# Optimization experiments

Hardware: AMD Instinct MI355X
Metric: run time of the kernel (lower is better)

The kernel has to match this reference:

```python
import jax, jax.numpy as jnp
import numpy as np

D_MODEL = 1024
NHEAD = 16
HEAD_DIM = D_MODEL // NHEAD
D_FF = 4096
EPS = 1e-5


def _layernorm(x, g, b):
    mu = jnp.mean(x, axis=-1, keepdims=True)
    var = jnp.mean((x - mu) ** 2, axis=-1, keepdims=True)
    return (x - mu) * jax.lax.rsqrt(var + EPS) * g + b


def setup_inputs() -> dict:
    key = jax.random.key(0)
    ks = jax.random.split(key, 13)
    s = 1.0 / np.sqrt(D_MODEL)
    sf = 1.0 / np.sqrt(D_FF)
    # weights stored as [in, out] (transposed torch Linear)
    return {
        "src": jax.random.normal(ks[0], (4, 2048, D_MODEL), jnp.float32),
        "Wq": jax.random.uniform(ks[1], (D_MODEL, D_MODEL), jnp.float32, -s, s),
        "bq": jnp.zeros((D_MODEL,), jnp.float32),
        "Wk": jax.random.uniform(ks[2], (D_MODEL, D_MODEL), jnp.float32, -s, s),
        "bk": jnp.zeros((D_MODEL,), jnp.float32),
        "Wv": jax.random.uniform(ks[3], (D_MODEL, D_MODEL), jnp.float32, -s, s),
        "bv": jnp.zeros((D_MODEL,), jnp.float32),
        "Wo": jax.random.uniform(ks[4], (D_MODEL, D_MODEL), jnp.float32, -s, s),
        "bo": jnp.zeros((D_MODEL,), jnp.float32),
        "W1": jax.random.uniform(ks[5], (D_MODEL, D_FF), jnp.float32, -s, s),
        "b1": jnp.zeros((D_FF,), jnp.float32),
        "W2": jax.random.uniform(ks[6], (D_FF, D_MODEL), jnp.float32, -sf, sf),
        "b2": jnp.zeros((D_MODEL,), jnp.float32),
        "g1": jnp.ones((D_MODEL,), jnp.float32),
        "be1": jnp.zeros((D_MODEL,), jnp.float32),
        "g2": jnp.ones((D_MODEL,), jnp.float32),
        "be2": jnp.zeros((D_MODEL,), jnp.float32),
    }


def reference(src, Wq, bq, Wk, bk, Wv, bv, Wo, bo, W1, b1, W2, b2, g1, be1, g2, be2):
    B, S, _ = src.shape
    scale = 1.0 / np.sqrt(HEAD_DIM)
    # project and split heads: [B, H, S, Dh]
    def heads(W, b):
        return (src @ W + b).reshape(B, S, NHEAD, HEAD_DIM).transpose(0, 2, 1, 3)
    Q, K, V = heads(Wq, bq), heads(Wk, bk), heads(Wv, bv)
    scores = jnp.einsum('bhqd,bhkd->bhqk', Q, K) * scale
    attn = jax.nn.softmax(scores, axis=-1)
    ctx = jnp.einsum('bhqk,bhkd->bhqd', attn, V)
    ctx = ctx.transpose(0, 2, 1, 3).reshape(B, S, D_MODEL)
    attn_out = ctx @ Wo + bo
    x = _layernorm(src + attn_out, g1, be1)
    ff = jax.nn.relu(x @ W1 + b1) @ W2 + b2
    return _layernorm(x + ff, g2, be2)
```

## Files before the change

kernel.cpp:

```cpp
#include <hip/hip_runtime.h>

typedef __attribute__((ext_vector_type(8))) short bf16x8;
typedef __attribute__((ext_vector_type(4))) float f32x4;
typedef unsigned short u16;
typedef unsigned int u32;

__device__ __forceinline__ u16 f2b(float f) {
  u32 u = __float_as_uint(f);
  u = (u + 0x7fffu + ((u >> 16) & 1u)) >> 16;
  return (u16)u;
}
__device__ __forceinline__ float b2f(u16 b) {
  return __uint_as_float(((u32)b) << 16);
}
__device__ __forceinline__ u32 cvtpk_bf16(float lo, float hi) {
  u32 r;
  asm("v_cvt_pk_bf16_f32 %0, %1, %2" : "=v"(r) : "v"(lo), "v"(hi));
  return r;
}
__device__ __forceinline__ void gload_lds16(const u16* g, u16* l) {
  __builtin_amdgcn_global_load_lds(
      (const __attribute__((address_space(1))) void*)g,
      (__attribute__((address_space(3))) void*)l, 16, 0, 0);
}

__global__ __launch_bounds__(256) void cvt_bf16(const float* __restrict__ in,
                                                u16* __restrict__ out, int n4) {
  int i = blockIdx.x * 256 + threadIdx.x;
  if (i >= n4) return;
  float4 v = ((const float4*)in)[i];
  ushort4 o;
  o.x = f2b(v.x); o.y = f2b(v.y); o.z = f2b(v.z); o.w = f2b(v.w);
  ((ushort4*)out)[i] = o;
}

__global__ __launch_bounds__(256) void transpose_w(const float* __restrict__ in,
                                                   u16* __restrict__ out,
                                                   int R, int C) {
  __shared__ float t[32][33];
  int tid = threadIdx.x, tx = tid & 31, ty = tid >> 5;
  int rb = blockIdx.y * 32, cb = blockIdx.x * 32;
  for (int i = 0; i < 4; i++)
    t[ty + i * 8][tx] = in[(size_t)(rb + ty + i * 8) * C + cb + tx];
  __syncthreads();
  for (int i = 0; i < 4; i++)
    out[(size_t)(cb + ty + i * 8) * R + rb + tx] = f2b(t[tx][ty + i * 8]);
}

__global__ __launch_bounds__(256) void concat3(const float* __restrict__ a,
                                               const float* __restrict__ b,
                                               const float* __restrict__ c,
                                               float* __restrict__ o) {
  int i = blockIdx.x * 256 + threadIdx.x;
  if (i >= 3072) return;
  o[i] = i < 1024 ? a[i] : (i < 2048 ? b[i - 1024] : c[i - 2048]);
}

__device__ __forceinline__ void stage_quarter(const u16* __restrict__ src,
                                              size_t rowbase, int K, int kcol,
                                              u16* dst, int c, int srow, int sg,
                                              int wid) {
  int row_ = c * 64 + srow;
  int gs_ = sg ^ (row_ & 7);
  gload_lds16(src + (rowbase + row_) * K + kcol + gs_ * 8,
              &dst[(c * 64 + wid * 8) * 64]);
}

template <bool PF>
__device__ __forceinline__ void tile_step(
    const u16* sAc, const u16* sBc, u16* sAn, u16* sBn,
    const u16* __restrict__ A, const u16* __restrict__ Bt, size_t abase,
    size_t bbase, int K, int Tn, int wm, int wn, int l16, int lq, int srow,
    int sg, int wid, f32x4 (&acc)[8][4]) {
  __syncthreads();
#pragma unroll
  for (int ks = 0; ks < 2; ++ks) {
    bf16x8 Bf[4], Af[4];
#pragma unroll
    for (int j = 0; j < 4; ++j) {
      int r = wn * 64 + j * 16 + l16;
      Bf[j] = *(const bf16x8*)&sBc[r * 64 + (((ks * 4 + lq) ^ (r & 7)) << 3)];
    }
#pragma unroll
    for (int i = 0; i < 4; ++i) {
      int r = wm * 128 + i * 16 + l16;
      Af[i] = *(const bf16x8*)&sAc[r * 64 + (((ks * 4 + lq) ^ (r & 7)) << 3)];
    }
    if (PF) {
      const u16* src = (ks == 0) ? A : Bt;
      size_t rb = (ks == 0) ? abase : bbase;
      u16* dst = (ks == 0) ? sAn : sBn;
      stage_quarter(src, rb, K, Tn * 64, dst, 0, srow, sg, wid);
      stage_quarter(src, rb, K, Tn * 64, dst, 1, srow, sg, wid);
    }
    __builtin_amdgcn_s_setprio(1);
#pragma unroll
    for (int i = 0; i < 4; ++i)
#pragma unroll
      for (int j = 0; j < 4; ++j)
        acc[i][j] = __builtin_amdgcn_mfma_f32_16x16x32_bf16(Af[i], Bf[j],
                                                            acc[i][j], 0, 0, 0);
    __builtin_amdgcn_s_setprio(0);
#pragma unroll
    for (int i = 0; i < 4; ++i) {
      int r = wm * 128 + 64 + i * 16 + l16;
      Af[i] = *(const bf16x8*)&sAc[r * 64 + (((ks * 4 + lq) ^ (r & 7)) << 3)];
    }
    if (PF) {
      const u16* src = (ks == 0) ? A : Bt;
      size_t rb = (ks == 0) ? abase : bbase;
      u16* dst = (ks == 0) ? sAn : sBn;
      stage_quarter(src, rb, K, Tn * 64, dst, 2, srow, sg, wid);
      stage_quarter(src, rb, K, Tn * 64, dst, 3, srow, sg, wid);
    }
    __builtin_amdgcn_s_setprio(1);
#pragma unroll
    for (int i = 0; i < 4; ++i)
#pragma unroll
      for (int j = 0; j < 4; ++j)
        acc[4 + i][j] = __builtin_amdgcn_mfma_f32_16x16x32_bf16(
            Af[i], Bf[j], acc[4 + i][j], 0, 0, 0);
    __builtin_amdgcn_s_setprio(0);
  }
}

template <int MODE>
__global__ __launch_bounds__(512, 1) void gemm256(const u16* __restrict__ A,
                                                  const u16* __restrict__ Bt,
                                                  const float* __restrict__ bias,
                                                  void* __restrict__ out,
                                                  int M, int N, int K,
                                                  float oscale) {
  __shared__ u16 sA0[256 * 64];
  __shared__ u16 sB0[256 * 64];
  __shared__ u16 sA1[256 * 64];
  __shared__ u16 sB1[256 * 64];
  const int tid = threadIdx.x, lane = tid & 63, wid = tid >> 6;
  const int l16 = lane & 15, lq = lane >> 4;
  const int wm = wid >> 2, wn = wid & 3;
  const size_t abase = (size_t)blockIdx.x * 256;
  const size_t bbase = (size_t)blockIdx.y * 256;
  const int srow = tid >> 3;
  const int sg = tid & 7;
  const int nt = K >> 6;

  f32x4 acc[8][4];
#pragma unroll
  for (int i = 0; i < 8; ++i)
#pragma unroll
    for (int j = 0; j < 4; ++j) acc[i][j] = (f32x4){0.f, 0.f, 0.f, 0.f};

#pragma unroll
  for (int c = 0; c < 4; ++c) {
    stage_quarter(A, abase, K, 0, sA0, c, srow, sg, wid);
    stage_quarter(Bt, bbase, K, 0, sB0, c, srow, sg, wid);
  }

  int T = 0;
  for (; T + 2 < nt; T += 2) {
    tile_step<true>(sA0, sB0, sA1, sB1, A, Bt, abase, bbase, K, T + 1, wm, wn,
                    l16, lq, srow, sg, wid, acc);
    tile_step<true>(sA1, sB1, sA0, sB0, A, Bt, abase, bbase, K, T + 2, wm, wn,
                    l16, lq, srow, sg, wid, acc);
  }
  tile_step<true>(sA0, sB0, sA1, sB1, A, Bt, abase, bbase, K, nt - 1, wm, wn,
                  l16, lq, srow, sg, wid, acc);
  tile_step<false>(sA1, sB1, sA0, sB0, A, Bt, abase, bbase, K, 0, wm, wn, l16,
                   lq, srow, sg, wid, acc);

  const int gmb = blockIdx.x * 256 + wm * 128;
  const int gnb = blockIdx.y * 256 + wn * 64;
#pragma unroll
  for (int i = 0; i < 8; ++i) {
    int gm0 = gmb + i * 16 + lq * 4;
#pragma unroll
    for (int j = 0; j < 4; ++j) {
      int gn = gnb + j * 16 + l16;
      float bv = bias[gn];
#pragma unroll
      for (int r = 0; r < 4; ++r) {
        float v = acc[i][j][r] + bv;
        ((u16*)out)[(size_t)(gm0 + r) * N + gn] = f2b(v > 0.f ? v : 0.f);
      }
    }
  }
}

template <bool PF>
__device__ __forceinline__ void tile_stepR(
    const u16* sAc, const u16* sBc, u16* sAn, u16* sBn,
    const u16* __restrict__ A, const u16* __restrict__ Bt, size_t abase,
    size_t bbase, int K, int Tn, int wm, int wn, int l16, int lq, int srow,
    int sg, int wid, f32x4 (&acc)[4][4]) {
  __syncthreads();
#pragma unroll
  for (int ks = 0; ks < 2; ++ks) {
    bf16x8 Bf[4], Af[4];
#pragma unroll
    for (int j = 0; j < 4; ++j) {
      int r = wn * 64 + j * 16 + l16;
      Bf[j] = *(const bf16x8*)&sBc[r * 64 + (((ks * 4 + lq) ^ (r & 7)) << 3)];
    }
#pragma unroll
    for (int i = 0; i < 4; ++i) {
      int r = wm * 64 + i * 16 + l16;
      Af[i] = *(const bf16x8*)&sAc[r * 64 + (((ks * 4 + lq) ^ (r & 7)) << 3)];
    }
    if (PF) {
      if (ks == 0) {
        stage_quarter(A, abase, K, Tn * 64, sAn, 0, srow, sg, wid);
        stage_quarter(A, abase, K, Tn * 64, sAn, 1, srow, sg, wid);
        stage_quarter(Bt, bbase, K, Tn * 64, sBn, 0, srow, sg, wid);
      } else {
        stage_quarter(Bt, bbase, K, Tn * 64, sBn, 1, srow, sg, wid);
        stage_quarter(Bt, bbase, K, Tn * 64, sBn, 2, srow, sg, wid);
        stage_quarter(Bt, bbase, K, Tn * 64, sBn, 3, srow, sg, wid);
      }
    }
    __builtin_amdgcn_s_setprio(1);
#pragma unroll
    for (int i = 0; i < 4; ++i)
#pragma unroll
      for (int j = 0; j < 4; ++j)
        acc[i][j] = __builtin_amdgcn_mfma_f32_16x16x32_bf16(Af[i], Bf[j],
                                                            acc[i][j], 0, 0, 0);
    __builtin_amdgcn_s_setprio(0);
  }
}

template <int MODE>
__global__ __launch_bounds__(512, 1) void gemmR(const u16* __restrict__ A,
                                                const u16* __restrict__ Bt,
                                                const float* __restrict__ bias,
                                                void* __restrict__ out,
                                                int M, int N, int K,
                                                float oscale) {
  __shared__ u16 sA0[128 * 64];
  __shared__ u16 sB0[256 * 64];
  __shared__ u16 sA1[128 * 64];
  __shared__ u16 sB1[256 * 64];
  const int tid = threadIdx.x, lane = tid & 63, wid = tid >> 6;
  const int l16 = lane & 15, lq = lane >> 4;
  const int wm = wid >> 2, wn = wid & 3;
  const size_t abase = (size_t)blockIdx.x * 128;
  const size_t bbase = (size_t)blockIdx.y * 256;
  const int srow = tid >> 3;
  const int sg = tid & 7;
  const int nt = K >> 6;

  f32x4 acc[4][4];
#pragma unroll
  for (int i = 0; i < 4; ++i)
#pragma unroll
    for (int j = 0; j < 4; ++j) acc[i][j] = (f32x4){0.f, 0.f, 0.f, 0.f};

#pragma unroll
  for (int c = 0; c < 2; ++c) stage_quarter(A, abase, K, 0, sA0, c, srow, sg, wid);
#pragma unroll
  for (int c = 0; c < 4; ++c) stage_quarter(Bt, bbase, K, 0, sB0, c, srow, sg, wid);

  int T = 0;
  for (; T + 2 < nt; T += 2) {
    tile_stepR<true>(sA0, sB0, sA1, sB1, A, Bt, abase, bbase, K, T + 1, wm, wn,
                     l16, lq, srow, sg, wid, acc);
    tile_stepR<true>(sA1, sB1, sA0, sB0, A, Bt, abase, bbase, K, T + 2, wm, wn,
                     l16, lq, srow, sg, wid, acc);
  }
  tile_stepR<true>(sA0, sB0, sA1, sB1, A, Bt, abase, bbase, K, nt - 1, wm, wn,
                   l16, lq, srow, sg, wid, acc);
  tile_stepR<false>(sA1, sB1, sA0, sB0, A, Bt, abase, bbase, K, 0, wm, wn, l16,
                    lq, srow, sg, wid, acc);

  const int gmb = blockIdx.x * 128 + wm * 64;
  const int gnb = blockIdx.y * 256 + wn * 64;
#pragma unroll
  for (int i = 0; i < 4; ++i) {
    int gm0 = gmb + i * 16 + lq * 4;
#pragma unroll
    for (int j = 0; j < 4; ++j) {
      int gn = gnb + j * 16 + l16;
      float bv = bias[gn];
      if constexpr (MODE == 1) {
#pragma unroll
        for (int r = 0; r < 4; ++r)
          ((u16*)out)[(size_t)(gm0 + r) * N + gn] = f2b(acc[i][j][r] + bv);
      } else {
        int sel = gn >> 10;
        int h = (gn & 1023) >> 6, d = gn & 63;
        int b = gm0 >> 11, s = gm0 & 2047;
        u16* o = (u16*)out + (size_t)sel * (8u << 20);
        if (sel == 2) {
          ushort4 w;
          w.x = f2b(acc[i][j][0] + bv);
          w.y = f2b(acc[i][j][1] + bv);
          w.z = f2b(acc[i][j][2] + bv);
          w.w = f2b(acc[i][j][3] + bv);
          *(ushort4*)(o + ((size_t)((b * 16 + h) * 64 + d)) * 2048 + s) = w;
        } else {
          float sc = (sel == 0) ? oscale : 1.f;
#pragma unroll
          for (int r = 0; r < 4; ++r)
            o[((size_t)(b * 16 + h) * 2048 + s + r) * 64 + d] =
                f2b((acc[i][j][r] + bv) * sc);
        }
      }
    }
  }
}

__global__ __launch_bounds__(256) void attn_fwd(const u16* __restrict__ Q,
                                                const u16* __restrict__ Kb,
                                                const u16* __restrict__ Vt,
                                                u16* __restrict__ ctx) {
  __shared__ u16 sK[64][64];
  __shared__ u16 sV[64][64];
  __shared__ u16 sP[4][16][72];
  const int tid = threadIdx.x, lane = tid & 63, wid = tid >> 6;
  const int l16 = lane & 15, lq = lane >> 4;
  const int bh = blockIdx.y, qt = blockIdx.x;
  const size_t base = (size_t)bh * (2048 * 64);
  const int xk = l16 & 7;

  bf16x8 qf[2];
  {
    int qrow = qt * 64 + wid * 16 + l16;
    qf[0] = *(const bf16x8*)(Q + base + (size_t)qrow * 64 + lq * 8);
    qf[1] = *(const bf16x8*)(Q + base + (size_t)qrow * 64 + 32 + lq * 8);
  }
  f32x4 o[4];
#pragma unroll
  for (int j = 0; j < 4; j++) o[j] = (f32x4){0.f, 0.f, 0.f, 0.f};
  float lrow = 0.f;

  const int srow_c = lane >> 3;
  const int sg8 = ((lane & 7) ^ srow_c) * 8;
  const int row0 = wid * 16 + srow_c, row1 = row0 + 8;
  const int wslot = (lane & 7) * 8;

  const u16* kp0 = Kb + base + (size_t)row0 * 64 + sg8;
  const u16* kp1 = Kb + base + (size_t)row1 * 64 + sg8;
  const u16* vp0 = Vt + base + (size_t)row0 * 2048 + sg8;
  const u16* vp1 = Vt + base + (size_t)row1 * 2048 + sg8;

  uint4 rk0 = *(const uint4*)kp0;
  uint4 rk1 = *(const uint4*)kp1;
  uint4 rv0 = *(const uint4*)vp0;
  uint4 rv1 = *(const uint4*)vp1;

  for (int kv0 = 0; kv0 < 2048; kv0 += 64) {
    __syncthreads();
    *(uint4*)&sK[row0][wslot] = rk0;
    *(uint4*)&sK[row1][wslot] = rk1;
    *(uint4*)&sV[row0][wslot] = rv0;
    *(uint4*)&sV[row1][wslot] = rv1;
    if (kv0 + 64 < 2048) {
      int kn = kv0 + 64;
      rk0 = *(const uint4*)(kp0 + (size_t)kn * 64);
      rk1 = *(const uint4*)(kp1 + (size_t)kn * 64);
      rv0 = *(const uint4*)(vp0 + kn);
      rv1 = *(const uint4*)(vp1 + kn);
    }
    __syncthreads();

    f32x4 sf[4];
#pragma unroll
    for (int j = 0; j < 4; j++) sf[j] = (f32x4){0.f, 0.f, 0.f, 0.f};
    __builtin_amdgcn_s_setprio(1);
#pragma unroll
    for (int ks = 0; ks < 2; ks++)
#pragma unroll
      for (int j = 0; j < 4; j++) {
        bf16x8 kf = *(const bf16x8*)&sK[j * 16 + l16][((ks * 4 + lq) ^ xk) * 8];
        sf[j] = __builtin_amdgcn_mfma_f32_16x16x32_bf16(kf, qf[ks], sf[j], 0, 0, 0);
      }
    __builtin_amdgcn_s_setprio(0);

    float rs = 0.f;
#pragma unroll
    for (int j = 0; j < 4; j++) {
      float p0 = __builtin_amdgcn_exp2f(sf[j][0]);
      float p1 = __builtin_amdgcn_exp2f(sf[j][1]);
      float p2 = __builtin_amdgcn_exp2f(sf[j][2]);
      float p3 = __builtin_amdgcn_exp2f(sf[j][3]);
      rs += (p0 + p1) + (p2 + p3);
      uint2 w;
      w.x = cvtpk_bf16(p0, p1);
      w.y = cvtpk_bf16(p2, p3);
      *(uint2*)&sP[wid][l16][j * 16 + lq * 4] = w;
    }
    rs += __shfl_xor(rs, 16);
    rs += __shfl_xor(rs, 32);
    lrow += rs;

    __builtin_amdgcn_s_setprio(1);
#pragma unroll
    for (int ks = 0; ks < 2; ks++) {
      bf16x8 pf = *(const bf16x8*)&sP[wid][l16][ks * 32 + lq * 8];
#pragma unroll
      for (int j = 0; j < 4; j++) {
        bf16x8 vf = *(const bf16x8*)&sV[j * 16 + l16][((ks * 4 + lq) ^ xk) * 8];
        o[j] = __builtin_amdgcn_mfma_f32_16x16x32_bf16(pf, vf, o[j], 0, 0, 0);
      }
    }
    __builtin_amdgcn_s_setprio(0);
  }

  float lval[4];
#pragma unroll
  for (int r = 0; r < 4; r++) lval[r] = 1.f / __shfl(lrow, lq * 4 + r);
  const int b = bh >> 4, h = bh & 15;
#pragma unroll
  for (int j = 0; j < 4; j++)
#pragma unroll
    for (int r = 0; r < 4; r++) {
      int srow = qt * 64 + wid * 16 + lq * 4 + r;
      int d = j * 16 + l16;
      ctx[((size_t)(b * 2048 + srow)) * 1024 + h * 64 + d] = f2b(o[j][r] * lval[r]);
    }
}

template <int A_BF16, int B_BF16, int WRITE_F32>
__global__ __launch_bounds__(256) void ln_res(const void* __restrict__ a,
                                              const void* __restrict__ bsrc,
                                              const float* __restrict__ g,
                                              const float* __restrict__ be,
                                              float* __restrict__ outf,
                                              u16* __restrict__ outb) {
  const int row = blockIdx.x, tid = threadIdx.x;
  const size_t off = (size_t)row * 1024 + tid * 4;
  float4 x;
  if constexpr (A_BF16) {
    ushort4 av = *(const ushort4*)((const u16*)a + off);
    x.x = b2f(av.x); x.y = b2f(av.y); x.z = b2f(av.z); x.w = b2f(av.w);
  } else {
    x = *(const float4*)((const float*)a + off);
  }
  if constexpr (B_BF16) {
    ushort4 bv = *(const ushort4*)((const u16*)bsrc + off);
    x.x += b2f(bv.x); x.y += b2f(bv.y); x.z += b2f(bv.z); x.w += b2f(bv.w);
  } else {
    float4 bb = *(const float4*)((const float*)bsrc + off);
    x.x += bb.x; x.y += bb.y; x.z += bb.z; x.w += bb.w;
  }
  float s = x.x + x.y + x.z + x.w;
  float s2 = x.x * x.x + x.y * x.y + x.z * x.z + x.w * x.w;
  for (int o = 1; o < 64; o <<= 1) {
    s += __shfl_xor(s, o);
    s2 += __shfl_xor(s2, o);
  }
  __shared__ float rbuf[8];
  int lane = tid & 63, wid = tid >> 6;
  if (lane == 0) { rbuf[wid] = s; rbuf[4 + wid] = s2; }
  __syncthreads();
  s = rbuf[0] + rbuf[1] + rbuf[2] + rbuf[3];
  s2 = rbuf[4] + rbuf[5] + rbuf[6] + rbuf[7];
  float mu = s * (1.f / 1024.f);
  float var = s2 * (1.f / 1024.f) - mu * mu;
  float rstd = rsqrtf(var + 1e-5f);
  int c = tid * 4;
  float y0 = (x.x - mu) * rstd * g[c + 0] + be[c + 0];
  float y1 = (x.y - mu) * rstd * g[c + 1] + be[c + 1];
  float y2 = (x.z - mu) * rstd * g[c + 2] + be[c + 2];
  float y3 = (x.w - mu) * rstd * g[c + 3] + be[c + 3];
  if constexpr (WRITE_F32) {
    float4 y; y.x = y0; y.y = y1; y.z = y2; y.w = y3;
    *(float4*)(outf + off) = y;
  } else {
    ushort4 yb;
    yb.x = f2b(y0); yb.y = f2b(y1); yb.z = f2b(y2); yb.w = f2b(y3);
    *(ushort4*)(outb + off) = yb;
  }
}

extern "C" void kernel_launch(void* const* d_in, const int* in_sizes, int n_in,
                              void* d_out, int out_size, void* d_ws, size_t ws_size,
                              hipStream_t stream) {
  const float* src = (const float*)d_in[0];
  const float* Wq = (const float*)d_in[1];
  const float* bq = (const float*)d_in[2];
  const float* Wk = (const float*)d_in[3];
  const float* bk = (const float*)d_in[4];
  const float* Wv = (const float*)d_in[5];
  const float* bv = (const float*)d_in[6];
  const float* Wo = (const float*)d_in[7];
  const float* bo = (const float*)d_in[8];
  const float* W1 = (const float*)d_in[9];
  const float* b1 = (const float*)d_in[10];
  const float* W2 = (const float*)d_in[11];
  const float* b2 = (const float*)d_in[12];
  const float* g1 = (const float*)d_in[13];
  const float* be1 = (const float*)d_in[14];
  const float* g2 = (const float*)d_in[15];
  const float* be2 = (const float*)d_in[16];
  float* out = (float*)d_out;
  char* ws = (char*)d_ws;
  const size_t MB = 1ull << 20;

  u16* XB    = (u16*)(ws + 0);
  u16* WQKVT = (u16*)(ws + 16 * MB);
  u16* WOT   = (u16*)(ws + 22 * MB);
  u16* W1T   = (u16*)(ws + 24 * MB);
  u16* W2T   = (u16*)(ws + 32 * MB);
  float* bqkv = (float*)(ws + 40 * MB);
  u16* Qb    = (u16*)(ws + 41 * MB);
  u16* Kbuf  = (u16*)(ws + 57 * MB);
  u16* Vt    = (u16*)(ws + 73 * MB);
  u16* CTX   = XB;
  u16* AO    = (u16*)(ws + 41 * MB);
  u16* H1    = (u16*)(ws + 57 * MB);
  u16* XBUF  = (u16*)(ws + 121 * MB);
  u16* FF    = XB;

  const float QSCALE = 0.125f * 1.44269504088896340736f;

  cvt_bf16<<<dim3(8192), dim3(256), 0, stream>>>(src, XB, 2097152);
  transpose_w<<<dim3(32, 32), dim3(256), 0, stream>>>(Wq, WQKVT, 1024, 1024);
  transpose_w<<<dim3(32, 32), dim3(256), 0, stream>>>(Wk, WQKVT + 1024 * 1024, 1024, 1024);
  transpose_w<<<dim3(32, 32), dim3(256), 0, stream>>>(Wv, WQKVT + 2048 * 1024, 1024, 1024);
  transpose_w<<<dim3(32, 32), dim3(256), 0, stream>>>(Wo, WOT, 1024, 1024);
  transpose_w<<<dim3(128, 32), dim3(256), 0, stream>>>(W1, W1T, 1024, 4096);
  transpose_w<<<dim3(32, 128), dim3(256), 0, stream>>>(W2, W2T, 4096, 1024);
  concat3<<<dim3(12), dim3(256), 0, stream>>>(bq, bk, bv, bqkv);

  gemmR<6><<<dim3(64, 12), dim3(512), 0, stream>>>(XB, WQKVT, bqkv, Qb,
                                                   8192, 3072, 1024, QSCALE);
  attn_fwd<<<dim3(32, 64), dim3(256), 0, stream>>>(Qb, Kbuf, Vt, CTX);
  gemmR<1><<<dim3(64, 4), dim3(512), 0, stream>>>(CTX, WOT, bo, AO,
                                                  8192, 1024, 1024, 1.0f);
  ln_res<0, 1, 0><<<dim3(8192), dim3(256), 0, stream>>>(src, AO, g1, be1, nullptr, XBUF);
  gemm256<2><<<dim3(32, 16), dim3(512), 0, stream>>>(XBUF, W1T, b1, H1,
                                                     8192, 4096, 1024, 1.0f);
  gemmR<1><<<dim3(64, 4), dim3(512), 0, stream>>>(H1, W2T, b2, FF,
                                                  8192, 1024, 4096, 1.0f);
  ln_res<1, 1, 1><<<dim3(8192), dim3(256), 0, stream>>>(XBUF, FF, g2, be2, out, nullptr);
}
```

Measured before the change: 367.6 us.

## Switch GEMMs to 4-stage BK=32 LDS pipeline with explicit vmcnt waits

```diff
diff --git a/kernel.cpp b/kernel.cpp
--- a/kernel.cpp
+++ b/kernel.cpp
@@ -22,6 +22,21 @@
   __builtin_amdgcn_global_load_lds(
       (const __attribute__((address_space(1))) void*)g,
       (__attribute__((address_space(3))) void*)l, 16, 0, 0);
+}
+template <int N>
+__device__ __forceinline__ void wait_vm_barrier() {
+  if constexpr (N == 8) asm volatile("s_waitcnt vmcnt(8)" ::: "memory");
+  else if constexpr (N == 6) asm volatile("s_waitcnt vmcnt(6)" ::: "memory");
+  else if constexpr (N == 4) asm volatile("s_waitcnt vmcnt(4)" ::: "memory");
+  else if constexpr (N == 3) asm volatile("s_waitcnt vmcnt(3)" ::: "memory");
+  else asm volatile("s_waitcnt vmcnt(0)" ::: "memory");
+  __builtin_amdgcn_s_barrier();
+  asm volatile("" ::: "memory");
+}
+__device__ __forceinline__ void align_barrier() {
+  asm volatile("" ::: "memory");
+  __builtin_amdgcn_s_barrier();
+  asm volatile("" ::: "memory");
 }
 
 __global__ __launch_bounds__(256) void cvt_bf16(const float* __restrict__ in,
@@ -56,72 +71,63 @@
   o[i] = i < 1024 ? a[i] : (i < 2048 ? b[i - 1024] : c[i - 2048]);
 }
 
-__device__ __forceinline__ void stage_quarter(const u16* __restrict__ src,
-                                              size_t rowbase, int K, int kcol,
-                                              u16* dst, int c, int srow, int sg,
-                                              int wid) {
-  int row_ = c * 64 + srow;
-  int gs_ = sg ^ (row_ & 7);
+__device__ __forceinline__ void stage32(const u16* __restrict__ src,
+                                        size_t rowbase, int K, int kcol,
+                                        u16* dst, int c, int tid) {
+  int row_ = c * 128 + (tid >> 2);
+  int gs_ = (tid & 3) ^ (row_ & 3);
   gload_lds16(src + (rowbase + row_) * K + kcol + gs_ * 8,
-              &dst[(c * 64 + wid * 8) * 64]);
+              &dst[(c * 128 + (tid >> 6) * 16) * 32]);
 }
 
 template <bool PF>
-__device__ __forceinline__ void tile_step(
-    const u16* sAc, const u16* sBc, u16* sAn, u16* sBn,
+__device__ __forceinline__ void tile32_256(
+    const u16* pA, const u16* pB, u16* wA, u16* wB,
     const u16* __restrict__ A, const u16* __restrict__ Bt, size_t abase,
-    size_t bbase, int K, int Tn, int wm, int wn, int l16, int lq, int srow,
-    int sg, int wid, f32x4 (&acc)[8][4]) {
-  __syncthreads();
-#pragma unroll
-  for (int ks = 0; ks < 2; ++ks) {
-    bf16x8 Bf[4], Af[4];
-#pragma unroll
-    for (int j = 0; j < 4; ++j) {
-      int r = wn * 64 + j * 16 + l16;
-      Bf[j] = *(const bf16x8*)&sBc[r * 64 + (((ks * 4 + lq) ^ (r & 7)) << 3)];
-    }
-#pragma unroll
-    for (int i = 0; i < 4; ++i) {
-      int r = wm * 128 + i * 16 + l16;
-      Af[i] = *(const bf16x8*)&sAc[r * 64 + (((ks * 4 + lq) ^ (r & 7)) << 3)];
-    }
-    if (PF) {
-      const u16* src = (ks == 0) ? A : Bt;
-      size_t rb = (ks == 0) ? abase : bbase;
-      u16* dst = (ks == 0) ? sAn : sBn;
-      stage_quarter(src, rb, K, Tn * 64, dst, 0, srow, sg, wid);
-      stage_quarter(src, rb, K, Tn * 64, dst, 1, srow, sg, wid);
-    }
-    __builtin_amdgcn_s_setprio(1);
-#pragma unroll
-    for (int i = 0; i < 4; ++i)
-#pragma unroll
-      for (int j = 0; j < 4; ++j)
-        acc[i][j] = __builtin_amdgcn_mfma_f32_16x16x32_bf16(Af[i], Bf[j],
-                                                            acc[i][j], 0, 0, 0);
-    __builtin_amdgcn_s_setprio(0);
-#pragma unroll
-    for (int i = 0; i < 4; ++i) {
-      int r = wm * 128 + 64 + i * 16 + l16;
-      Af[i] = *(const bf16x8*)&sAc[r * 64 + (((ks * 4 + lq) ^ (r & 7)) << 3)];
-    }
-    if (PF) {
-      const u16* src = (ks == 0) ? A : Bt;
-      size_t rb = (ks == 0) ? abase : bbase;
-      u16* dst = (ks == 0) ? sAn : sBn;
-      stage_quarter(src, rb, K, Tn * 64, dst, 2, srow, sg, wid);
-      stage_quarter(src, rb, K, Tn * 64, dst, 3, srow, sg, wid);
-    }
-    __builtin_amdgcn_s_setprio(1);
-#pragma unroll
-    for (int i = 0; i < 4; ++i)
-#pragma unroll
-      for (int j = 0; j < 4; ++j)
-        acc[4 + i][j] = __builtin_amdgcn_mfma_f32_16x16x32_bf16(
-            Af[i], Bf[j], acc[4 + i][j], 0, 0, 0);
-    __builtin_amdgcn_s_setprio(0);
-  }
+    size_t bbase, int K, int Tn, int wm, int wn, int l16, int lq, int tid,
+    f32x4 (&acc)[8][4]) {
+  bf16x8 Bf[4], Af[4];
+#pragma unroll
+  for (int j = 0; j < 4; ++j) {
+    int r = wn * 64 + j * 16 + l16;
+    Bf[j] = *(const bf16x8*)&pB[r * 32 + ((lq ^ (r & 3)) << 3)];
+  }
+#pragma unroll
+  for (int i = 0; i < 4; ++i) {
+    int r = wm * 128 + i * 16 + l16;
+    Af[i] = *(const bf16x8*)&pA[r * 32 + ((lq ^ (r & 3)) << 3)];
+  }
+  if (PF) {
+    stage32(A, abase, K, Tn * 32, wA, 0, tid);
+    stage32(A, abase, K, Tn * 32, wA, 1, tid);
+  }
+  align_barrier();
+  __builtin_amdgcn_s_setprio(1);
+#pragma unroll
+  for (int i = 0; i < 4; ++i)
+#pragma unroll
+    for (int j = 0; j < 4; ++j)
+      acc[i][j] = __builtin_amdgcn_mfma_f32_16x16x32_bf16(Af[i], Bf[j],
+                                                          acc[i][j], 0, 0, 0);
+  __builtin_amdgcn_s_setprio(0);
+#pragma unroll
+  for (int i = 0; i < 4; ++i) {
+    int r = wm * 128 + 64 + i * 16 + l16;
+    Af[i] = *(const bf16x8*)&pA[r * 32 + ((lq ^ (r & 3)) << 3)];
+  }
+  if (PF) {
+    stage32(Bt, bbase, K, Tn * 32, wB, 0, tid);
+    stage32(Bt, bbase, K, Tn * 32, wB, 1, tid);
+  }
+  align_barrier();
+  __builtin_amdgcn_s_setprio(1);
+#pragma unroll
+  for (int i = 0; i < 4; ++i)
+#pragma unroll
+    for (int j = 0; j < 4; ++j)
+      acc[4 + i][j] = __builtin_amdgcn_mfma_f32_16x16x32_bf16(
+          Af[i], Bf[j], acc[4 + i][j], 0, 0, 0);
+  __builtin_amdgcn_s_setprio(0);
 }
 
 template <int MODE>
@@ -131,18 +137,14 @@
                                                   void* __restrict__ out,
                                                   int M, int N, int K,
                                                   float oscale) {
-  __shared__ u16 sA0[256 * 64];
-  __shared__ u16 sB0[256 * 64];
-  __shared__ u16 sA1[256 * 64];
-  __shared__ u16 sB1[256 * 64];
+  __shared__ u16 sA0[256 * 32], sA1[256 * 32], sA2[256 * 32], sA3[256 * 32];
+  __shared__ u16 sB0[256 * 32], sB1[256 * 32], sB2[256 * 32], sB3[256 * 32];
   const int tid = threadIdx.x, lane = tid & 63, wid = tid >> 6;
   const int l16 = lane & 15, lq = lane >> 4;
   const int wm = wid >> 2, wn = wid & 3;
   const size_t abase = (size_t)blockIdx.x * 256;
   const size_t bbase = (size_t)blockIdx.y * 256;
-  const int srow = tid >> 3;
-  const int sg = tid & 7;
-  const int nt = K >> 6;
+  const int nt = K >> 5;
 
   f32x4 acc[8][4];
 #pragma unroll
@@ -150,23 +152,35 @@
 #pragma unroll
     for (int j = 0; j < 4; ++j) acc[i][j] = (f32x4){0.f, 0.f, 0.f, 0.f};
 
-#pragma unroll
-  for (int c = 0; c < 4; ++c) {
-    stage_quarter(A, abase, K, 0, sA0, c, srow, sg, wid);
-    stage_quarter(Bt, bbase, K, 0, sB0, c, srow, sg, wid);
-  }
-
-  int T = 0;
-  for (; T + 2 < nt; T += 2) {
-    tile_step<true>(sA0, sB0, sA1, sB1, A, Bt, abase, bbase, K, T + 1, wm, wn,
-                    l16, lq, srow, sg, wid, acc);
-    tile_step<true>(sA1, sB1, sA0, sB0, A, Bt, abase, bbase, K, T + 2, wm, wn,
-                    l16, lq, srow, sg, wid, acc);
-  }
-  tile_step<true>(sA0, sB0, sA1, sB1, A, Bt, abase, bbase, K, nt - 1, wm, wn,
-                  l16, lq, srow, sg, wid, acc);
-  tile_step<false>(sA1, sB1, sA0, sB0, A, Bt, abase, bbase, K, 0, wm, wn, l16,
-                   lq, srow, sg, wid, acc);
+  stage32(A, abase, K, 0, sA0, 0, tid);
+  stage32(A, abase, K, 0, sA0, 1, tid);
+  stage32(Bt, bbase, K, 0, sB0, 0, tid);
+  stage32(Bt, bbase, K, 0, sB0, 1, tid);
+  stage32(A, abase, K, 32, sA1, 0, tid);
+  stage32(A, abase, K, 32, sA1, 1, tid);
+  stage32(Bt, bbase, K, 32, sB1, 0, tid);
+  stage32(Bt, bbase, K, 32, sB1, 1, tid);
+  stage32(A, abase, K, 64, sA2, 0, tid);
+  stage32(A, abase, K, 64, sA2, 1, tid);
+  stage32(Bt, bbase, K, 64, sB2, 0, tid);
+  stage32(Bt, bbase, K, 64, sB2, 1, tid);
+
+  u16 *A0 = sA0, *A1 = sA1, *A2 = sA2, *A3 = sA3;
+  u16 *B0 = sB0, *B1 = sB1, *B2 = sB2, *B3 = sB3;
+  for (int T = 0; T < nt; ++T) {
+    if (T < nt - 2) wait_vm_barrier<8>();
+    else if (T == nt - 2) wait_vm_barrier<4>();
+    else wait_vm_barrier<0>();
+    if (T + 3 < nt)
+      tile32_256<true>(A0, B0, A3, B3, A, Bt, abase, bbase, K, T + 3, wm, wn,
+                       l16, lq, tid, acc);
+    else
+      tile32_256<false>(A0, B0, A3, B3, A, Bt, abase, bbase, K, 0, wm, wn, l16,
+                        lq, tid, acc);
+    u16* t;
+    t = A0; A0 = A1; A1 = A2; A2 = A3; A3 = t;
+    t = B0; B0 = B1; B1 = B2; B2 = B3; B3 = t;
+  }
 
   const int gmb = blockIdx.x * 256 + wm * 128;
   const int gnb = blockIdx.y * 256 + wn * 64;
@@ -187,45 +201,36 @@
 }
 
 template <bool PF>
-__device__ __forceinline__ void tile_stepR(
-    const u16* sAc, const u16* sBc, u16* sAn, u16* sBn,
+__device__ __forceinline__ void tile32_R(
+    const u16* pA, const u16* pB, u16* wA, u16* wB,
     const u16* __restrict__ A, const u16* __restrict__ Bt, size_t abase,
-    size_t bbase, int K, int Tn, int wm, int wn, int l16, int lq, int srow,
-    int sg, int wid, f32x4 (&acc)[4][4]) {
-  __syncthreads();
-#pragma unroll
-  for (int ks = 0; ks < 2; ++ks) {
-    bf16x8 Bf[4], Af[4];
-#pragma unroll
-    for (int j = 0; j < 4; ++j) {
-      int r = wn * 64 + j * 16 + l16;
-      Bf[j] = *(const bf16x8*)&sBc[r * 64 + (((ks * 4 + lq) ^ (r & 7)) << 3)];
-    }
-#pragma unroll
-    for (int i = 0; i < 4; ++i) {
-      int r = wm * 64 + i * 16 + l16;
-      Af[i] = *(const bf16x8*)&sAc[r * 64 + (((ks * 4 + lq) ^ (r & 7)) << 3)];
-    }
-    if (PF) {
-      if (ks == 0) {
-        stage_quarter(A, abase, K, Tn * 64, sAn, 0, srow, sg, wid);
-        stage_quarter(A, abase, K, Tn * 64, sAn, 1, srow, sg, wid);
-        stage_quarter(Bt, bbase, K, Tn * 64, sBn, 0, srow, sg, wid);
-      } else {
-        stage_quarter(Bt, bbase, K, Tn * 64, sBn, 1, srow, sg, wid);
-        stage_quarter(Bt, bbase, K, Tn * 64, sBn, 2, srow, sg, wid);
-        stage_quarter(Bt, bbase, K, Tn * 64, sBn, 3, srow, sg, wid);
-      }
-    }
-    __builtin_amdgcn_s_setprio(1);
-#pragma unroll
-    for (int i = 0; i < 4; ++i)
-#pragma unroll
-      for (int j = 0; j < 4; ++j)
-        acc[i][j] = __builtin_amdgcn_mfma_f32_16x16x32_bf16(Af[i], Bf[j],
-                                                            acc[i][j], 0, 0, 0);
-    __builtin_amdgcn_s_setprio(0);
-  }
+    size_t bbase, int K, int Tn, int wm, int wn, int l16, int lq, int tid,
+    f32x4 (&acc)[4][4]) {
+  bf16x8 Bf[4], Af[4];
+#pragma unroll
+  for (int j = 0; j < 4; ++j) {
+    int r = wn * 64 + j * 16 + l16;
+    Bf[j] = *(const bf16x8*)&pB[r * 32 + ((lq ^ (r & 3)) << 3)];
+  }
+#pragma unroll
+  for (int i = 0; i < 4; ++i) {
+    int r = wm * 64 + i * 16 + l16;
+    Af[i] = *(const bf16x8*)&pA[r * 32 + ((lq ^ (r & 3)) << 3)];
+  }
+  if (PF) {
+    stage32(A, abase, K, Tn * 32, wA, 0, tid);
+    stage32(Bt, bbase, K, Tn * 32, wB, 0, tid);
+    stage32(Bt, bbase, K, Tn * 32, wB, 1, tid);
+  }
+  align_barrier();
+  __builtin_amdgcn_s_setprio(1);
+#pragma unroll
+  for (int i = 0; i < 4; ++i)
+#pragma unroll
+    for (int j = 0; j < 4; ++j)
+      acc[i][j] = __builtin_amdgcn_mfma_f32_16x16x32_bf16(Af[i], Bf[j],
+                                                          acc[i][j], 0, 0, 0);
+  __builtin_amdgcn_s_setprio(0);
 }
 
 template <int MODE>
@@ -235,18 +240,14 @@
                                                 void* __restrict__ out,
                                                 int M, int N, int K,
                                                 float oscale) {
-  __shared__ u16 sA0[128 * 64];
-  __shared__ u16 sB0[256 * 64];
-  __shared__ u16 sA1[128 * 64];
-  __shared__ u16 sB1[256 * 64];
+  __shared__ u16 sA0[128 * 32], sA1[128 * 32], sA2[128 * 32], sA3[128 * 32];
+  __shared__ u16 sB0[256 * 32], sB1[256 * 32], sB2[256 * 32], sB3[256 * 32];
   const int tid = threadIdx.x, lane = tid & 63, wid = tid >> 6;
   const int l16 = lane & 15, lq = lane >> 4;
   const int wm = wid >> 2, wn = wid & 3;
   const size_t abase = (size_t)blockIdx.x * 128;
   const size_t bbase = (size_t)blockIdx.y * 256;
-  const int srow = tid >> 3;
-  const int sg = tid & 7;
-  const int nt = K >> 6;
+  const int nt = K >> 5;
 
   f32x4 acc[4][4];
 #pragma unroll
@@ -254,22 +255,32 @@
 #pragma unroll
     for (int j = 0; j < 4; ++j) acc[i][j] = (f32x4){0.f, 0.f, 0.f, 0.f};
 
-#pragma unroll
-  for (int c = 0; c < 2; ++c) stage_quarter(A, abase, K, 0, sA0, c, srow, sg, wid);
-#pragma unroll
-  for (int c = 0; c < 4; ++c) stage_quarter(Bt, bbase, K, 0, sB0, c, srow, sg, wid);
-
-  int T = 0;
-  for (; T + 2 < nt; T += 2) {
-    tile_stepR<true>(sA0, sB0, sA1, sB1, A, Bt, abase, bbase, K, T + 1, wm, wn,
-                     l16, lq, srow, sg, wid, acc);
-    tile_stepR<true>(sA1, sB1, sA0, sB0, A, Bt, abase, bbase, K, T + 2, wm, wn,
-                     l16, lq, srow, sg, wid, acc);
-  }
-  tile_stepR<true>(sA0, sB0, sA1, sB1, A, Bt, abase, bbase, K, nt - 1, wm, wn,
-                   l16, lq, srow, sg, wid, acc);
-  tile_stepR<false>(sA1, sB1, sA0, sB0, A, Bt, abase, bbase, K, 0, wm, wn, l16,
-                    lq, srow, sg, wid, acc);
+  stage32(A, abase, K, 0, sA0, 0, tid);
+  stage32(Bt, bbase, K, 0, sB0, 0, tid);
+  stage32(Bt, bbase, K, 0, sB0, 1, tid);
+  stage32(A, abase, K, 32, sA1, 0, tid);
+  stage32(Bt, bbase, K, 32, sB1, 0, tid);
+  stage32(Bt, bbase, K, 32, sB1, 1, tid);
+  stage32(A, abase, K, 64, sA2, 0, tid);
+  stage32(Bt, bbase, K, 64, sB2, 0, tid);
+  stage32(Bt, bbase, K, 64, sB2, 1, tid);
+
+  u16 *A0 = sA0, *A1 = sA1, *A2 = sA2, *A3 = sA3;
+  u16 *B0 = sB0, *B1 = sB1, *B2 = sB2, *B3 = sB3;
+  for (int T = 0; T < nt; ++T) {
+    if (T < nt - 2) wait_vm_barrier<6>();
+    else if (T == nt - 2) wait_vm_barrier<3>();
+    else wait_vm_barrier<0>();
+    if (T + 3 < nt)
+      tile32_R<true>(A0, B0, A3, B3, A, Bt, abase, bbase, K, T + 3, wm, wn,
+                     l16, lq, tid, acc);
+    else
+      tile32_R<false>(A0, B0, A3, B3, A, Bt, abase, bbase, K, 0, wm, wn, l16,
+                      lq, tid, acc);
+    u16* t;
+    t = A0; A0 = A1; A1 = A2; A2 = A3; A3 = t;
+    t = B0; B0 = B1; B1 = B2; B2 = B3; B3 = t;
+  }
 
   const int gmb = blockIdx.x * 128 + wm * 64;
   const int gnb = blockIdx.y * 256 + wn * 64;
```

New measurement: 928.8 us. +152.7%, slower.

## Restructure GEMM main loop into 4-phase schedule with partial vmcnt barriers

Applied to the files above, without the earlier changes.

```diff
diff --git a/kernel.cpp b/kernel.cpp
--- a/kernel.cpp
+++ b/kernel.cpp
@@ -22,6 +22,19 @@
   __builtin_amdgcn_global_load_lds(
       (const __attribute__((address_space(1))) void*)g,
       (__attribute__((address_space(3))) void*)l, 16, 0, 0);
+}
+template <int N>
+__device__ __forceinline__ void vm_barrier() {
+  if constexpr (N == 4) asm volatile("s_waitcnt vmcnt(4)" ::: "memory");
+  else if constexpr (N == 2) asm volatile("s_waitcnt vmcnt(2)" ::: "memory");
+  else asm volatile("s_waitcnt vmcnt(0)" ::: "memory");
+  __builtin_amdgcn_s_barrier();
+  asm volatile("" ::: "memory");
+}
+__device__ __forceinline__ void plain_barrier() {
+  asm volatile("" ::: "memory");
+  __builtin_amdgcn_s_barrier();
+  asm volatile("" ::: "memory");
 }
 
 __global__ __launch_bounds__(256) void cvt_bf16(const float* __restrict__ in,
@@ -67,61 +80,112 @@
 }
 
 template <bool PF>
-__device__ __forceinline__ void tile_step(
-    const u16* sAc, const u16* sBc, u16* sAn, u16* sBn,
+__device__ __forceinline__ void tile8(
+    const u16* cA, const u16* cB, u16* nA, u16* nB,
     const u16* __restrict__ A, const u16* __restrict__ Bt, size_t abase,
     size_t bbase, int K, int Tn, int wm, int wn, int l16, int lq, int srow,
     int sg, int wid, f32x4 (&acc)[8][4]) {
-  __syncthreads();
-#pragma unroll
-  for (int ks = 0; ks < 2; ++ks) {
-    bf16x8 Bf[4], Af[4];
+  bf16x8 Bf[4][2];
+  bf16x8 Af[2][2];
+
+  vm_barrier<2>();
+#pragma unroll
+  for (int ks = 0; ks < 2; ++ks)
 #pragma unroll
     for (int j = 0; j < 4; ++j) {
       int r = wn * 64 + j * 16 + l16;
-      Bf[j] = *(const bf16x8*)&sBc[r * 64 + (((ks * 4 + lq) ^ (r & 7)) << 3)];
-    }
-#pragma unroll
-    for (int i = 0; i < 4; ++i) {
-      int r = wm * 128 + i * 16 + l16;
-      Af[i] = *(const bf16x8*)&sAc[r * 64 + (((ks * 4 + lq) ^ (r & 7)) << 3)];
-    }
-    if (PF) {
-      const u16* src = (ks == 0) ? A : Bt;
-      size_t rb = (ks == 0) ? abase : bbase;
-      u16* dst = (ks == 0) ? sAn : sBn;
-      stage_quarter(src, rb, K, Tn * 64, dst, 0, srow, sg, wid);
-      stage_quarter(src, rb, K, Tn * 64, dst, 1, srow, sg, wid);
-    }
-    __builtin_amdgcn_s_setprio(1);
-#pragma unroll
-    for (int i = 0; i < 4; ++i)
+      Bf[j][ks] = *(const bf16x8*)&cB[r * 64 + (((ks * 4 + lq) ^ (r & 7)) << 3)];
+    }
+#pragma unroll
+  for (int ks = 0; ks < 2; ++ks)
+#pragma unroll
+    for (int i = 0; i < 2; ++i) {
+      int r = wm * 128 + 0 * 32 + i * 16 + l16;
+      Af[i][ks] = *(const bf16x8*)&cA[r * 64 + (((ks * 4 + lq) ^ (r & 7)) << 3)];
+    }
+  if (PF) {
+    stage_quarter(Bt, bbase, K, Tn * 64, nB, 0, srow, sg, wid);
+    stage_quarter(Bt, bbase, K, Tn * 64, nB, 1, srow, sg, wid);
+  }
+  __builtin_amdgcn_s_setprio(1);
+#pragma unroll
+  for (int ks = 0; ks < 2; ++ks)
+#pragma unroll
+    for (int i = 0; i < 2; ++i)
 #pragma unroll
       for (int j = 0; j < 4; ++j)
-        acc[i][j] = __builtin_amdgcn_mfma_f32_16x16x32_bf16(Af[i], Bf[j],
+        acc[i][j] = __builtin_amdgcn_mfma_f32_16x16x32_bf16(Af[i][ks], Bf[j][ks],
                                                             acc[i][j], 0, 0, 0);
-    __builtin_amdgcn_s_setprio(0);
-#pragma unroll
-    for (int i = 0; i < 4; ++i) {
-      int r = wm * 128 + 64 + i * 16 + l16;
-      Af[i] = *(const bf16x8*)&sAc[r * 64 + (((ks * 4 + lq) ^ (r & 7)) << 3)];
-    }
-    if (PF) {
-      const u16* src = (ks == 0) ? A : Bt;
-      size_t rb = (ks == 0) ? abase : bbase;
-      u16* dst = (ks == 0) ? sAn : sBn;
-      stage_quarter(src, rb, K, Tn * 64, dst, 2, srow, sg, wid);
-      stage_quarter(src, rb, K, Tn * 64, dst, 3, srow, sg, wid);
-    }
-    __builtin_amdgcn_s_setprio(1);
-#pragma unroll
-    for (int i = 0; i < 4; ++i)
+  __builtin_amdgcn_s_setprio(0);
+
+  plain_barrier();
+#pragma unroll
+  for (int ks = 0; ks < 2; ++ks)
+#pragma unroll
+    for (int i = 0; i < 2; ++i) {
+      int r = wm * 128 + 1 * 32 + i * 16 + l16;
+      Af[i][ks] = *(const bf16x8*)&cA[r * 64 + (((ks * 4 + lq) ^ (r & 7)) << 3)];
+    }
+  if (PF) {
+    stage_quarter(Bt, bbase, K, Tn * 64, nB, 2, srow, sg, wid);
+    stage_quarter(Bt, bbase, K, Tn * 64, nB, 3, srow, sg, wid);
+  }
+  __builtin_amdgcn_s_setprio(1);
+#pragma unroll
+  for (int ks = 0; ks < 2; ++ks)
+#pragma unroll
+    for (int i = 0; i < 2; ++i)
+#pragma unroll
+      for (int j = 0; j < 4; ++j)
+        acc[2 + i][j] = __builtin_amdgcn_mfma_f32_16x16x32_bf16(
+            Af[i][ks], Bf[j][ks], acc[2 + i][j], 0, 0, 0);
+  __builtin_amdgcn_s_setprio(0);
+
+  if (PF) vm_barrier<4>(); else vm_barrier<0>();
+#pragma unroll
+  for (int ks = 0; ks < 2; ++ks)
+#pragma unroll
+    for (int i = 0; i < 2; ++i) {
+      int r = wm * 128 + 2 * 32 + i * 16 + l16;
+      Af[i][ks] = *(const bf16x8*)&cA[r * 64 + (((ks * 4 + lq) ^ (r & 7)) << 3)];
+    }
+  if (PF) {
+    stage_quarter(A, abase, K, Tn * 64, nA, 0, srow, sg, wid);
+    stage_quarter(A, abase, K, Tn * 64, nA, 2, srow, sg, wid);
+  }
+  __builtin_amdgcn_s_setprio(1);
+#pragma unroll
+  for (int ks = 0; ks < 2; ++ks)
+#pragma unroll
+    for (int i = 0; i < 2; ++i)
 #pragma unroll
       for (int j = 0; j < 4; ++j)
         acc[4 + i][j] = __builtin_amdgcn_mfma_f32_16x16x32_bf16(
-            Af[i], Bf[j], acc[4 + i][j], 0, 0, 0);
-    __builtin_amdgcn_s_setprio(0);
-  }
+            Af[i][ks], Bf[j][ks], acc[4 + i][j], 0, 0, 0);
+  __builtin_amdgcn_s_setprio(0);
+
+  plain_barrier();
+#pragma unroll
+  for (int ks = 0; ks < 2; ++ks)
+#pragma unroll
+    for (int i = 0; i < 2; ++i) {
+      int r = wm * 128 + 3 * 32 + i * 16 + l16;
+      Af[i][ks] = *(const bf16x8*)&cA[r * 64 + (((ks * 4 + lq) ^ (r & 7)) << 3)];
+    }
+  if (PF) {
+    stage_quarter(A, abase, K, Tn * 64, nA, 1, srow, sg, wid);
+    stage_quarter(A, abase, K, Tn * 64, nA, 3, srow, sg, wid);
+  }
+  __builtin_amdgcn_s_setprio(1);
+#pragma unroll
+  for (int ks = 0; ks < 2; ++ks)
+#pragma unroll
+    for (int i = 0; i < 2; ++i)
+#pragma unroll
+      for (int j = 0; j < 4; ++j)
+        acc[6 + i][j] = __builtin_amdgcn_mfma_f32_16x16x32_bf16(
+            Af[i][ks], Bf[j][ks], acc[6 + i][j], 0, 0, 0);
+  __builtin_amdgcn_s_setprio(0);
 }
 
 template <int MODE>
@@ -150,23 +214,26 @@
 #pragma unroll
     for (int j = 0; j < 4; ++j) acc[i][j] = (f32x4){0.f, 0.f, 0.f, 0.f};
 
-#pragma unroll
-  for (int c = 0; c < 4; ++c) {
-    stage_quarter(A, abase, K, 0, sA0, c, srow, sg, wid);
-    stage_quarter(Bt, bbase, K, 0, sB0, c, srow, sg, wid);
-  }
+  stage_quarter(Bt, bbase, K, 0, sB0, 0, srow, sg, wid);
+  stage_quarter(Bt, bbase, K, 0, sB0, 1, srow, sg, wid);
+  stage_quarter(Bt, bbase, K, 0, sB0, 2, srow, sg, wid);
+  stage_quarter(Bt, bbase, K, 0, sB0, 3, srow, sg, wid);
+  stage_quarter(A, abase, K, 0, sA0, 0, srow, sg, wid);
+  stage_quarter(A, abase, K, 0, sA0, 2, srow, sg, wid);
+  stage_quarter(A, abase, K, 0, sA0, 1, srow, sg, wid);
+  stage_quarter(A, abase, K, 0, sA0, 3, srow, sg, wid);
 
   int T = 0;
   for (; T + 2 < nt; T += 2) {
-    tile_step<true>(sA0, sB0, sA1, sB1, A, Bt, abase, bbase, K, T + 1, wm, wn,
-                    l16, lq, srow, sg, wid, acc);
-    tile_step<true>(sA1, sB1, sA0, sB0, A, Bt, abase, bbase, K, T + 2, wm, wn,
-                    l16, lq, srow, sg, wid, acc);
-  }
-  tile_step<true>(sA0, sB0, sA1, sB1, A, Bt, abase, bbase, K, nt - 1, wm, wn,
-                  l16, lq, srow, sg, wid, acc);
-  tile_step<false>(sA1, sB1, sA0, sB0, A, Bt, abase, bbase, K, 0, wm, wn, l16,
-                   lq, srow, sg, wid, acc);
+    tile8<true>(sA0, sB0, sA1, sB1, A, Bt, abase, bbase, K, T + 1, wm, wn, l16,
+                lq, srow, sg, wid, acc);
+    tile8<true>(sA1, sB1, sA0, sB0, A, Bt, abase, bbase, K, T + 2, wm, wn, l16,
+                lq, srow, sg, wid, acc);
+  }
+  tile8<true>(sA0, sB0, sA1, sB1, A, Bt, abase, bbase, K, nt - 1, wm, wn, l16,
+              lq, srow, sg, wid, acc);
+  tile8<false>(sA1, sB1, sA0, sB0, A, Bt, abase, bbase, K, 0, wm, wn, l16, lq,
+               srow, sg, wid, acc);
 
   const int gmb = blockIdx.x * 256 + wm * 128;
   const int gnb = blockIdx.y * 256 + wn * 64;
```

New measurement: 372.1 us. About the same (+1.2%).
